# Performance work log

Hardware: AMD Instinct MI355X
Metric: run time of the kernel (lower is better)

Reference implementation:

```python
import jax, jax.numpy as jnp
import numpy as np

B, NB, T, C, H, FW, TW = 4, 64, 512, 256, 8, 8, 8
HD = C // H
SCALE = HD ** -0.5
EPS = 1e-5


def setup_inputs() -> dict:
    key = jax.random.key(0)
    ks = jax.random.split(key, 12)
    inpt = jax.random.normal(ks[0], (B, NB, T, C), jnp.float32)
    perm_n = jax.vmap(lambda k: jax.random.permutation(k, NB))(jax.random.split(ks[1], B)).astype(jnp.int32)
    perm_t = jax.vmap(lambda k: jax.random.permutation(k, T))(jax.random.split(ks[2], B)).astype(jnp.int32)
    w = lambda k, shp: (jax.random.normal(k, shp, jnp.float32) * 0.02)
    return {
        "inpt": inpt, "perm_n": perm_n, "perm_t": perm_t,
        "ln_g": jnp.ones((C,), jnp.float32), "ln_b": jnp.zeros((C,), jnp.float32),
        "Wq": w(ks[3], (C, C)), "bq": jnp.zeros((C,), jnp.float32),
        "Wk": w(ks[4], (C, C)), "bk": jnp.zeros((C,), jnp.float32),
        "Wv": w(ks[5], (C, C)), "bv": jnp.zeros((C,), jnp.float32),
        "Wp": w(ks[6], (C, C)), "bp": jnp.zeros((C,), jnp.float32),
    }


def _layernorm(x, g, b):
    m = x.mean(-1, keepdims=True)
    v = ((x - m) ** 2).mean(-1, keepdims=True)
    return (x - m) * jax.lax.rsqrt(v + EPS) * g + b


def reference(inpt, perm_n, perm_t, ln_g, ln_b, Wq, bq, Wk, bk, Wv, bv, Wp, bp):
    x = _layernorm(inpt, ln_g, ln_b)  # (B, NB, T, C)

    # per-batch shuffle: gather along N then along T
    shuffled = jax.vmap(lambda xb, pn, pt: xb[pn][:, pt])(x, perm_n, perm_t)

    # window partition -> (B*NB/FW*T/TW, FW*TW, C)
    win = shuffled.reshape(B, NB // FW, FW, T // TW, TW, C)
    win = win.transpose(0, 1, 3, 2, 4, 5).reshape(-1, FW * TW, C)

    def heads(y):  # (Bw, L, C) -> (Bw, H, L, HD)
        return y.reshape(y.shape[0], y.shape[1], H, HD).transpose(0, 2, 1, 3)

    q = heads(win @ Wq.T + bq) * SCALE
    k = heads(win @ Wk.T + bk)
    v = heads(win @ Wv.T + bv)

    attn = jax.nn.softmax(jnp.einsum('bhqd,bhkd->bhqk', q, k), axis=-1)
    o = jnp.einsum('bhqk,bhkd->bhqd', attn, v)
    o = o.transpose(0, 2, 1, 3).reshape(-1, FW * TW, C)
    o = o @ Wp.T + bp

    # window reverse -> (B, NB, T, C)
    y = o.reshape(B, NB // FW, T // TW, FW, TW, C)
    y = y.transpose(0, 1, 3, 2, 4, 5).reshape(B, NB, T, C)

    # scatter reverse == gather with inverse permutations
    inv_n = jnp.argsort(perm_n, axis=-1)
    inv_t = jnp.argsort(perm_t, axis=-1)
    unshuf = jax.vmap(lambda yb, qn, qt: yb[:, qt][qn])(y, inv_n, inv_t)

    return inpt + unshuf
```

## Files before the change

kernel.cpp:

```cpp
#include <hip/hip_runtime.h>

typedef __attribute__((ext_vector_type(4))) float f32x4;
typedef __attribute__((ext_vector_type(8))) short bf16x8;

#define EPS_ 1e-5f
#define QSC 0.25503639409729144f

#define CBASE 16384
#define CHUNK 6144
#define KOFF 2048
#define VTOFF 4096
#define LDS_US 40960
#define LDS_BYTES (LDS_US * 2)

__device__ __forceinline__ int swzx(int r, int c) { return r * 256 + (c ^ ((r & 7) << 3)); }
__device__ __forceinline__ int swzq(int r, int c) { return r * 32 + (c ^ (((r >> 1) & 3) << 3)); }
__device__ __forceinline__ int swzp(int r, int c) { return r * 64 + (c ^ ((r & 7) << 3)); }

__device__ __forceinline__ unsigned int pack2(float a, float b) {
  union { float f; unsigned int u; } ua, ub;
  ua.f = a; ub.f = b;
  unsigned int ra = (ua.u + 0x7FFFu + ((ua.u >> 16) & 1u)) >> 16;
  unsigned int rb = (ub.u + 0x7FFFu + ((ub.u >> 16) & 1u)) & 0xFFFF0000u;
  return ra | rb;
}
__device__ __forceinline__ uint2 pack4(f32x4 v) {
  uint2 o; o.x = pack2(v[0], v[1]); o.y = pack2(v[2], v[3]); return o;
}
__device__ __forceinline__ unsigned short f2b(float f) {
  union { float f; unsigned int u; } c; c.f = f;
  return (unsigned short)((c.u + 0x7FFFu + ((c.u >> 16) & 1u)) >> 16);
}

__global__ __launch_bounds__(256) void k0_cvt(const float* __restrict__ w0,
                                              const float* __restrict__ w1,
                                              const float* __restrict__ w2,
                                              const float* __restrict__ w3,
                                              unsigned short* __restrict__ dst) {
  int idx = blockIdx.x * 256 + threadIdx.x;
  const float* s = (blockIdx.y == 0) ? w0 : (blockIdx.y == 1) ? w1 : (blockIdx.y == 2) ? w2 : w3;
  dst[blockIdx.y * 65536 + idx] = f2b(s[idx]);
}

__global__ __launch_bounds__(256, 2) void ka_fused(
    const unsigned short* __restrict__ Wall,
    const float* __restrict__ ln_g, const float* __restrict__ ln_b,
    const int* __restrict__ pn, const int* __restrict__ pt,
    const float* __restrict__ bq, const float* __restrict__ bk,
    const float* __restrict__ bv, const float* __restrict__ bp,
    const float* __restrict__ inpt, float* __restrict__ out) {
  extern __shared__ unsigned short lds[];

  const int tid = threadIdx.x;
  const int wv = tid >> 6, lane = tid & 63, quad = lane >> 4, l15 = lane & 15;
  const int w = blockIdx.x;
  const int b = w >> 9, nbb = (w >> 6) & 7, tbb = w & 63;
  const f32x4 z4 = {0.f, 0.f, 0.f, 0.f};

  {
    const float4 gg = ((const float4*)ln_g)[lane];
    const float4 bb = ((const float4*)ln_b)[lane];
    #pragma unroll
    for (int ii = 0; ii < 2; ++ii) {
      const int nloc = wv * 2 + ii;
      const int spn = pn[(b << 6) + (nbb << 3) + nloc];
      const float* rowbase = inpt + (size_t)((b << 6) + spn) * 512 * 256;
      float4 v[8];
      #pragma unroll
      for (int i = 0; i < 8; ++i) {
        const int spt = pt[(b << 9) + (tbb << 3) + i];
        v[i] = ((const float4*)(rowbase + (size_t)spt * 256))[lane];
      }
      #pragma unroll
      for (int i = 0; i < 8; ++i) {
        float s = v[i].x + v[i].y + v[i].z + v[i].w;
        float ss = v[i].x * v[i].x + v[i].y * v[i].y + v[i].z * v[i].z + v[i].w * v[i].w;
        #pragma unroll
        for (int m = 1; m < 64; m <<= 1) { s += __shfl_xor(s, m); ss += __shfl_xor(ss, m); }
        const float mean = s * (1.0f / 256.0f);
        const float rs = rsqrtf(ss * (1.0f / 256.0f) - mean * mean + EPS_);
        ushort4 o;
        o.x = f2b((v[i].x - mean) * rs * gg.x + bb.x);
        o.y = f2b((v[i].y - mean) * rs * gg.y + bb.y);
        o.z = f2b((v[i].z - mean) * rs * gg.z + bb.z);
        o.w = f2b((v[i].w - mean) * rs * gg.w + bb.w);
        const int row = nloc * 8 + i;
        *(ushort4*)(lds + swzx(row, lane * 4)) = o;
      }
    }
  }
  __syncthreads();

  const unsigned short* Wq = Wall;
  const unsigned short* Wk = Wall + 65536;
  const unsigned short* Wv_ = Wall + 131072;
  const unsigned short* Wp = Wall + 196608;
  unsigned short* chunk = lds + CBASE + wv * CHUNK;

  uint2 opk[2][2][4];

  #pragma unroll
  for (int hh = 0; hh < 2; ++hh) {
    const int h = (wv << 1) + hh;

    f32x4 qa[2][4], ka_[2][4], va[4][2];
    #pragma unroll
    for (int m2 = 0; m2 < 2; ++m2)
      #pragma unroll
      for (int nt = 0; nt < 4; ++nt) { qa[m2][nt] = z4; ka_[m2][nt] = z4; }
    #pragma unroll
    for (int mt = 0; mt < 4; ++mt)
      #pragma unroll
      for (int m2 = 0; m2 < 2; ++m2) va[mt][m2] = z4;

    #pragma unroll
    for (int ks = 0; ks < 8; ++ks) {
      bf16x8 bx[4];
      #pragma unroll
      for (int nt = 0; nt < 4; ++nt)
        bx[nt] = *(const bf16x8*)(lds + swzx(nt * 16 + l15, ks * 32 + quad * 8));
      #pragma unroll
      for (int m2 = 0; m2 < 2; ++m2) {
        const int wrow = (h * 32 + m2 * 16 + l15) * 256 + ks * 32 + quad * 8;
        bf16x8 wq8 = *(const bf16x8*)(Wq + wrow);
        bf16x8 wk8 = *(const bf16x8*)(Wk + wrow);
        bf16x8 wv8 = *(const bf16x8*)(Wv_ + wrow);
        #pragma unroll
        for (int nt = 0; nt < 4; ++nt) {
          qa[m2][nt] = __builtin_amdgcn_mfma_f32_16x16x32_bf16(wq8, bx[nt], qa[m2][nt], 0, 0, 0);
          ka_[m2][nt] = __builtin_amdgcn_mfma_f32_16x16x32_bf16(wk8, bx[nt], ka_[m2][nt], 0, 0, 0);
          va[nt][m2] = __builtin_amdgcn_mfma_f32_16x16x32_bf16(bx[nt], wv8, va[nt][m2], 0, 0, 0);
        }
      }
    }

    #pragma unroll
    for (int m2 = 0; m2 < 2; ++m2) {
      float4 bq4 = ((const float4*)(bq + h * 32 + m2 * 16))[quad];
      float4 bk4 = ((const float4*)(bk + h * 32 + m2 * 16))[quad];
      #pragma unroll
      for (int nt = 0; nt < 4; ++nt) {
        f32x4 qv, kv;
        qv[0] = (qa[m2][nt][0] + bq4.x) * QSC; kv[0] = ka_[m2][nt][0] + bk4.x;
        qv[1] = (qa[m2][nt][1] + bq4.y) * QSC; kv[1] = ka_[m2][nt][1] + bk4.y;
        qv[2] = (qa[m2][nt][2] + bq4.z) * QSC; kv[2] = ka_[m2][nt][2] + bk4.z;
        qv[3] = (qa[m2][nt][3] + bq4.w) * QSC; kv[3] = ka_[m2][nt][3] + bk4.w;
        const int r = nt * 16 + l15, c = m2 * 16 + quad * 4;
        *(uint2*)(chunk + swzq(r, c)) = pack4(qv);
        *(uint2*)(chunk + KOFF + swzq(r, c)) = pack4(kv);
      }
      const float bvv = bv[h * 32 + m2 * 16 + l15];
      #pragma unroll
      for (int mt = 0; mt < 4; ++mt) {
        f32x4 vv;
        vv[0] = va[mt][m2][0] + bvv; vv[1] = va[mt][m2][1] + bvv;
        vv[2] = va[mt][m2][2] + bvv; vv[3] = va[mt][m2][3] + bvv;
        *(uint2*)(chunk + VTOFF + swzp(m2 * 16 + l15, mt * 16 + quad * 4)) = pack4(vv);
      }
    }

    bf16x8 qf[4], kf[4];
    #pragma unroll
    for (int i = 0; i < 4; ++i) {
      qf[i] = *(const bf16x8*)(chunk + swzq(i * 16 + l15, quad * 8));
      kf[i] = *(const bf16x8*)(chunk + KOFF + swzq(i * 16 + l15, quad * 8));
    }
    f32x4 st[4][4];
    #pragma unroll
    for (int mtk = 0; mtk < 4; ++mtk)
      #pragma unroll
      for (int ntq = 0; ntq < 4; ++ntq)
        st[mtk][ntq] = __builtin_amdgcn_mfma_f32_16x16x32_bf16(kf[mtk], qf[ntq], z4, 0, 0, 0);

    float inv[4];
    #pragma unroll
    for (int ntq = 0; ntq < 4; ++ntq) {
      float tot = 0.f;
      #pragma unroll
      for (int mtk = 0; mtk < 4; ++mtk)
        #pragma unroll
        for (int r = 0; r < 4; ++r) {
          const float e = __builtin_amdgcn_exp2f(st[mtk][ntq][r]);
          st[mtk][ntq][r] = e; tot += e;
        }
      tot += __shfl_xor(tot, 16);
      tot += __shfl_xor(tot, 32);
      inv[ntq] = 1.0f / tot;
    }
    #pragma unroll
    for (int ntq = 0; ntq < 4; ++ntq)
      #pragma unroll
      for (int mtk = 0; mtk < 4; ++mtk) {
        f32x4 pv;
        pv[0] = st[mtk][ntq][0] * inv[ntq]; pv[1] = st[mtk][ntq][1] * inv[ntq];
        pv[2] = st[mtk][ntq][2] * inv[ntq]; pv[3] = st[mtk][ntq][3] * inv[ntq];
        *(uint2*)(chunk + swzp(ntq * 16 + l15, mtk * 16 + quad * 4)) = pack4(pv);
      }

    f32x4 oa[2][4];
    #pragma unroll
    for (int m2 = 0; m2 < 2; ++m2)
      #pragma unroll
      for (int ntq = 0; ntq < 4; ++ntq) oa[m2][ntq] = z4;
    #pragma unroll
    for (int kk = 0; kk < 2; ++kk) {
      bf16x8 pb[4], vf[2];
      #pragma unroll
      for (int ntq = 0; ntq < 4; ++ntq)
        pb[ntq] = *(const bf16x8*)(chunk + swzp(ntq * 16 + l15, kk * 32 + quad * 8));
      #pragma unroll
      for (int m2 = 0; m2 < 2; ++m2)
        vf[m2] = *(const bf16x8*)(chunk + VTOFF + swzp(m2 * 16 + l15, kk * 32 + quad * 8));
      #pragma unroll
      for (int m2 = 0; m2 < 2; ++m2)
        #pragma unroll
        for (int ntq = 0; ntq < 4; ++ntq)
          oa[m2][ntq] = __builtin_amdgcn_mfma_f32_16x16x32_bf16(vf[m2], pb[ntq], oa[m2][ntq], 0, 0, 0);
    }
    #pragma unroll
    for (int m2 = 0; m2 < 2; ++m2)
      #pragma unroll
      for (int ntq = 0; ntq < 4; ++ntq) opk[hh][m2][ntq] = pack4(oa[m2][ntq]);
  }

  __syncthreads();
  #pragma unroll
  for (int hh = 0; hh < 2; ++hh)
    #pragma unroll
    for (int m2 = 0; m2 < 2; ++m2)
      #pragma unroll
      for (int ntq = 0; ntq < 4; ++ntq)
        *(uint2*)(lds + swzx(ntq * 16 + l15, ((wv * 2 + hh) * 32 + m2 * 16 + quad * 4))) =
            opk[hh][m2][ntq];
  __syncthreads();

  f32x4 pacc[4][4];
  #pragma unroll
  for (int m4 = 0; m4 < 4; ++m4)
    #pragma unroll
    for (int nto = 0; nto < 4; ++nto) pacc[m4][nto] = z4;
  #pragma unroll
  for (int ks = 0; ks < 8; ++ks) {
    bf16x8 ob[4];
    #pragma unroll
    for (int nto = 0; nto < 4; ++nto)
      ob[nto] = *(const bf16x8*)(lds + swzx(nto * 16 + l15, ks * 32 + quad * 8));
    #pragma unroll
    for (int m4 = 0; m4 < 4; ++m4) {
      bf16x8 wp8 = *(const bf16x8*)(Wp + (wv * 64 + m4 * 16 + l15) * 256 + ks * 32 + quad * 8);
      #pragma unroll
      for (int nto = 0; nto < 4; ++nto)
        pacc[m4][nto] = __builtin_amdgcn_mfma_f32_16x16x32_bf16(wp8, ob[nto], pacc[m4][nto], 0, 0, 0);
    }
  }

  int toff[4];
  #pragma unroll
  for (int nto = 0; nto < 4; ++nto) {
    const int tok = nto * 16 + l15;
    const int n = (nbb << 3) + (tok >> 3), t = (tbb << 3) + (tok & 7);
    toff[nto] = (((b << 6) + pn[(b << 6) + n]) * 512 + pt[(b << 9) + t]) * 256;
  }
  #pragma unroll
  for (int m4 = 0; m4 < 4; ++m4) {
    float4 bp4 = ((const float4*)(bp + wv * 64 + m4 * 16))[quad];
    #pragma unroll
    for (int nto = 0; nto < 4; ++nto) {
      const int off = toff[nto] + wv * 64 + m4 * 16 + quad * 4;
      float4 iv = *(const float4*)(inpt + off);
      float4 o;
      o.x = iv.x + pacc[m4][nto][0] + bp4.x;
      o.y = iv.y + pacc[m4][nto][1] + bp4.y;
      o.z = iv.z + pacc[m4][nto][2] + bp4.z;
      o.w = iv.w + pacc[m4][nto][3] + bp4.w;
      *(float4*)(out + off) = o;
    }
  }
}

extern "C" void kernel_launch(void* const* d_in, const int* in_sizes, int n_in,
                              void* d_out, int out_size, void* d_ws, size_t ws_size,
                              hipStream_t stream) {
  const float* inpt = (const float*)d_in[0];
  const int* perm_n = (const int*)d_in[1];
  const int* perm_t = (const int*)d_in[2];
  const float* ln_g = (const float*)d_in[3];
  const float* ln_b = (const float*)d_in[4];
  const float* Wq = (const float*)d_in[5];
  const float* bq = (const float*)d_in[6];
  const float* Wk = (const float*)d_in[7];
  const float* bk = (const float*)d_in[8];
  const float* Wv = (const float*)d_in[9];
  const float* bv = (const float*)d_in[10];
  const float* Wp = (const float*)d_in[11];
  const float* bp = (const float*)d_in[12];
  float* out = (float*)d_out;

  unsigned short* Wall = (unsigned short*)d_ws;

  (void)hipFuncSetAttribute((const void*)ka_fused,
                            hipFuncAttributeMaxDynamicSharedMemorySize, LDS_BYTES);

  k0_cvt<<<dim3(256, 4), 256, 0, stream>>>(Wq, Wk, Wv, Wp, Wall);
  ka_fused<<<2048, 256, LDS_BYTES, stream>>>(Wall, ln_g, ln_b, perm_n, perm_t,
                                             bq, bk, bv, bp, inpt, out);
}
```

Before: 456.5 us.

## Keep attention operands in registers via bpermute instead of LDS staging

```diff
diff --git a/kernel.cpp b/kernel.cpp
--- a/kernel.cpp
+++ b/kernel.cpp
@@ -6,16 +6,9 @@
 #define EPS_ 1e-5f
 #define QSC 0.25503639409729144f
 
-#define CBASE 16384
-#define CHUNK 6144
-#define KOFF 2048
-#define VTOFF 4096
-#define LDS_US 40960
-#define LDS_BYTES (LDS_US * 2)
+#define LDS_BYTES 32768
 
 __device__ __forceinline__ int swzx(int r, int c) { return r * 256 + (c ^ ((r & 7) << 3)); }
-__device__ __forceinline__ int swzq(int r, int c) { return r * 32 + (c ^ (((r >> 1) & 3) << 3)); }
-__device__ __forceinline__ int swzp(int r, int c) { return r * 64 + (c ^ ((r & 7) << 3)); }
 
 __device__ __forceinline__ unsigned int pack2(float a, float b) {
   union { float f; unsigned int u; } ua, ub;
@@ -30,6 +23,25 @@
 __device__ __forceinline__ unsigned short f2b(float f) {
   union { float f; unsigned int u; } c; c.f = f;
   return (unsigned short)((c.u + 0x7FFFu + ((c.u >> 16) & 1u)) >> 16);
+}
+
+__device__ __forceinline__ bf16x8 xform(f32x4 A0, f32x4 A1, int ae, int ao, bool hi) {
+  int P0 = (int)pack2(A0[0], A0[1]), P1 = (int)pack2(A0[2], A0[3]);
+  int P2 = (int)pack2(A1[0], A1[1]), P3 = (int)pack2(A1[2], A1[3]);
+  int e0 = __builtin_amdgcn_ds_bpermute(ae, P0);
+  int e1 = __builtin_amdgcn_ds_bpermute(ae, P1);
+  int e2 = __builtin_amdgcn_ds_bpermute(ae, P2);
+  int e3 = __builtin_amdgcn_ds_bpermute(ae, P3);
+  int o0 = __builtin_amdgcn_ds_bpermute(ao, P0);
+  int o1 = __builtin_amdgcn_ds_bpermute(ao, P1);
+  int o2 = __builtin_amdgcn_ds_bpermute(ao, P2);
+  int o3 = __builtin_amdgcn_ds_bpermute(ao, P3);
+  union { bf16x8 v; int u[4]; } r;
+  r.u[0] = hi ? e2 : e0;
+  r.u[1] = hi ? e3 : e1;
+  r.u[2] = hi ? o2 : o0;
+  r.u[3] = hi ? o3 : o1;
+  return r.v;
 }
 
 __global__ __launch_bounds__(256) void k0_cvt(const float* __restrict__ w0,
@@ -42,7 +54,7 @@
   dst[blockIdx.y * 65536 + idx] = f2b(s[idx]);
 }
 
-__global__ __launch_bounds__(256, 2) void ka_fused(
+__global__ __launch_bounds__(256, 3) void ka_fused(
     const unsigned short* __restrict__ Wall,
     const float* __restrict__ ln_g, const float* __restrict__ ln_b,
     const int* __restrict__ pn, const int* __restrict__ pt,
@@ -56,6 +68,10 @@
   const int w = blockIdx.x;
   const int b = w >> 9, nbb = (w >> 6) & 7, tbb = w & 63;
   const f32x4 z4 = {0.f, 0.f, 0.f, 0.f};
+
+  const int ae = ((((quad << 1) & 3) << 4) + l15) << 2;
+  const int ao = (((((quad << 1) + 1) & 3) << 4) + l15) << 2;
+  const bool hi = lane >= 32;
 
   {
     const float4 gg = ((const float4*)ln_g)[lane];
@@ -95,7 +111,6 @@
   const unsigned short* Wk = Wall + 65536;
   const unsigned short* Wv_ = Wall + 131072;
   const unsigned short* Wp = Wall + 196608;
-  unsigned short* chunk = lds + CBASE + wv * CHUNK;
 
   uint2 opk[2][2][4];
 
@@ -136,91 +151,66 @@
 
     #pragma unroll
     for (int m2 = 0; m2 < 2; ++m2) {
-      float4 bq4 = ((const float4*)(bq + h * 32 + m2 * 16))[quad];
-      float4 bk4 = ((const float4*)(bk + h * 32 + m2 * 16))[quad];
+      const float4 bq4 = ((const float4*)(bq + h * 32 + m2 * 16))[quad];
+      const float4 bk4 = ((const float4*)(bk + h * 32 + m2 * 16))[quad];
+      const float bvv = bv[h * 32 + m2 * 16 + l15];
       #pragma unroll
       for (int nt = 0; nt < 4; ++nt) {
-        f32x4 qv, kv;
-        qv[0] = (qa[m2][nt][0] + bq4.x) * QSC; kv[0] = ka_[m2][nt][0] + bk4.x;
-        qv[1] = (qa[m2][nt][1] + bq4.y) * QSC; kv[1] = ka_[m2][nt][1] + bk4.y;
-        qv[2] = (qa[m2][nt][2] + bq4.z) * QSC; kv[2] = ka_[m2][nt][2] + bk4.z;
-        qv[3] = (qa[m2][nt][3] + bq4.w) * QSC; kv[3] = ka_[m2][nt][3] + bk4.w;
-        const int r = nt * 16 + l15, c = m2 * 16 + quad * 4;
-        *(uint2*)(chunk + swzq(r, c)) = pack4(qv);
-        *(uint2*)(chunk + KOFF + swzq(r, c)) = pack4(kv);
-      }
-      const float bvv = bv[h * 32 + m2 * 16 + l15];
-      #pragma unroll
-      for (int mt = 0; mt < 4; ++mt) {
-        f32x4 vv;
-        vv[0] = va[mt][m2][0] + bvv; vv[1] = va[mt][m2][1] + bvv;
-        vv[2] = va[mt][m2][2] + bvv; vv[3] = va[mt][m2][3] + bvv;
-        *(uint2*)(chunk + VTOFF + swzp(m2 * 16 + l15, mt * 16 + quad * 4)) = pack4(vv);
-      }
-    }
-
-    bf16x8 qf[4], kf[4];
-    #pragma unroll
-    for (int i = 0; i < 4; ++i) {
-      qf[i] = *(const bf16x8*)(chunk + swzq(i * 16 + l15, quad * 8));
-      kf[i] = *(const bf16x8*)(chunk + KOFF + swzq(i * 16 + l15, quad * 8));
-    }
-    f32x4 st[4][4];
-    #pragma unroll
-    for (int mtk = 0; mtk < 4; ++mtk)
-      #pragma unroll
-      for (int ntq = 0; ntq < 4; ++ntq)
-        st[mtk][ntq] = __builtin_amdgcn_mfma_f32_16x16x32_bf16(kf[mtk], qf[ntq], z4, 0, 0, 0);
-
-    float inv[4];
-    #pragma unroll
-    for (int ntq = 0; ntq < 4; ++ntq) {
-      float tot = 0.f;
-      #pragma unroll
-      for (int mtk = 0; mtk < 4; ++mtk)
+        qa[m2][nt][0] = (qa[m2][nt][0] + bq4.x) * QSC;
+        qa[m2][nt][1] = (qa[m2][nt][1] + bq4.y) * QSC;
+        qa[m2][nt][2] = (qa[m2][nt][2] + bq4.z) * QSC;
+        qa[m2][nt][3] = (qa[m2][nt][3] + bq4.w) * QSC;
+        ka_[m2][nt][0] += bk4.x; ka_[m2][nt][1] += bk4.y;
+        ka_[m2][nt][2] += bk4.z; ka_[m2][nt][3] += bk4.w;
+        va[nt][m2][0] += bvv; va[nt][m2][1] += bvv;
+        va[nt][m2][2] += bvv; va[nt][m2][3] += bvv;
+      }
+    }
+
+    bf16x8 qf[4], kf[4], vf[2][2];
+    #pragma unroll
+    for (int i = 0; i < 4; ++i) qf[i] = xform(qa[0][i], qa[1][i], ae, ao, hi);
+    #pragma unroll
+    for (int i = 0; i < 4; ++i) kf[i] = xform(ka_[0][i], ka_[1][i], ae, ao, hi);
+    #pragma unroll
+    for (int kk = 0; kk < 2; ++kk)
+      #pragma unroll
+      for (int m2 = 0; m2 < 2; ++m2)
+        vf[kk][m2] = xform(va[2 * kk][m2], va[2 * kk + 1][m2], ae, ao, hi);
+
+    float tot[4] = {0.f, 0.f, 0.f, 0.f};
+    bf16x8 pb[2][4];
+    #pragma unroll
+    for (int kk = 0; kk < 2; ++kk)
+      #pragma unroll
+      for (int ntq = 0; ntq < 4; ++ntq) {
+        f32x4 s0 = __builtin_amdgcn_mfma_f32_16x16x32_bf16(kf[2 * kk], qf[ntq], z4, 0, 0, 0);
+        f32x4 s1 = __builtin_amdgcn_mfma_f32_16x16x32_bf16(kf[2 * kk + 1], qf[ntq], z4, 0, 0, 0);
         #pragma unroll
         for (int r = 0; r < 4; ++r) {
-          const float e = __builtin_amdgcn_exp2f(st[mtk][ntq][r]);
-          st[mtk][ntq][r] = e; tot += e;
+          s0[r] = __builtin_amdgcn_exp2f(s0[r]); tot[ntq] += s0[r];
+          s1[r] = __builtin_amdgcn_exp2f(s1[r]); tot[ntq] += s1[r];
         }
-      tot += __shfl_xor(tot, 16);
-      tot += __shfl_xor(tot, 32);
-      inv[ntq] = 1.0f / tot;
-    }
-    #pragma unroll
-    for (int ntq = 0; ntq < 4; ++ntq)
-      #pragma unroll
-      for (int mtk = 0; mtk < 4; ++mtk) {
-        f32x4 pv;
-        pv[0] = st[mtk][ntq][0] * inv[ntq]; pv[1] = st[mtk][ntq][1] * inv[ntq];
-        pv[2] = st[mtk][ntq][2] * inv[ntq]; pv[3] = st[mtk][ntq][3] * inv[ntq];
-        *(uint2*)(chunk + swzp(ntq * 16 + l15, mtk * 16 + quad * 4)) = pack4(pv);
-      }
-
-    f32x4 oa[2][4];
+        pb[kk][ntq] = xform(s0, s1, ae, ao, hi);
+      }
+    float inv[4];
+    #pragma unroll
+    for (int ntq = 0; ntq < 4; ++ntq) {
+      float t = tot[ntq];
+      t += __shfl_xor(t, 16);
+      t += __shfl_xor(t, 32);
+      inv[ntq] = 1.0f / t;
+    }
+
     #pragma unroll
     for (int m2 = 0; m2 < 2; ++m2)
       #pragma unroll
-      for (int ntq = 0; ntq < 4; ++ntq) oa[m2][ntq] = z4;
-    #pragma unroll
-    for (int kk = 0; kk < 2; ++kk) {
-      bf16x8 pb[4], vf[2];
-      #pragma unroll
-      for (int ntq = 0; ntq < 4; ++ntq)
-        pb[ntq] = *(const bf16x8*)(chunk + swzp(ntq * 16 + l15, kk * 32 + quad * 8));
-      #pragma unroll
-      for (int m2 = 0; m2 < 2; ++m2)
-        vf[m2] = *(const bf16x8*)(chunk + VTOFF + swzp(m2 * 16 + l15, kk * 32 + quad * 8));
-      #pragma unroll
-      for (int m2 = 0; m2 < 2; ++m2)
-        #pragma unroll
-        for (int ntq = 0; ntq < 4; ++ntq)
-          oa[m2][ntq] = __builtin_amdgcn_mfma_f32_16x16x32_bf16(vf[m2], pb[ntq], oa[m2][ntq], 0, 0, 0);
-    }
-    #pragma unroll
-    for (int m2 = 0; m2 < 2; ++m2)
-      #pragma unroll
-      for (int ntq = 0; ntq < 4; ++ntq) opk[hh][m2][ntq] = pack4(oa[m2][ntq]);
+      for (int ntq = 0; ntq < 4; ++ntq) {
+        f32x4 oa = __builtin_amdgcn_mfma_f32_16x16x32_bf16(vf[0][m2], pb[0][ntq], z4, 0, 0, 0);
+        oa = __builtin_amdgcn_mfma_f32_16x16x32_bf16(vf[1][m2], pb[1][ntq], oa, 0, 0, 0);
+        oa[0] *= inv[ntq]; oa[1] *= inv[ntq]; oa[2] *= inv[ntq]; oa[3] *= inv[ntq];
+        opk[hh][m2][ntq] = pack4(oa);
+      }
   }
 
   __syncthreads();
```

After: 514.8 us. 1.13x slower.
